# Performance work log

Measured on AMD Instinct MI355X. Metric: run time of the kernel, lower is better.

The kernel has to match this reference:

```python
import jax, jax.numpy as jnp
import numpy as np

N = 38333          # poi_len == number of graph nodes (forced by fc_layer input dim)
E = 38333 * 32     # edges, avg degree 32
VOCAB = 400 + 38333 + 1083   # cat_len + poi_len + user_len = 39816
EMB = (128 - 3) // 2         # 62
IN_DIM = EMB * 2 + 3         # 127
SLOPE = 0.01                 # LeakyReLU default negative_slope


def setup_inputs() -> dict:
    key = jax.random.key(0)
    ks = jax.random.split(key, 20)
    ids = jax.random.randint(ks[0], (N, 2), 0, VOCAB).astype(jnp.float32)
    feats = jax.random.uniform(ks[1], (N, 3), dtype=jnp.float32)
    x = jnp.concatenate([ids, feats], axis=1)                      # [N,5]
    edge_index = jax.random.randint(ks[2], (2, E), 0, N, dtype=jnp.int64)
    s = 0.05
    inp = {
        "x": x,
        "edge_index": edge_index,
        "emb": jax.random.normal(ks[3], (VOCAB, EMB), jnp.float32) * s,
        "W1": jax.random.normal(ks[4], (IN_DIM, 64), jnp.float32) * s,
        "b1": jnp.zeros((64,), jnp.float32),
        "W2": jax.random.normal(ks[5], (64, 32), jnp.float32) * s,
        "b2": jnp.zeros((32,), jnp.float32),
        "W3": jax.random.normal(ks[6], (32, 32), jnp.float32) * s,
        "b3": jnp.zeros((32,), jnp.float32),
        "W4": jax.random.normal(ks[7], (32, 32), jnp.float32) * s,
        "b4": jnp.zeros((32,), jnp.float32),
        "W5": jax.random.normal(ks[8], (32, 1), jnp.float32) * s,
        "b5": jnp.zeros((1,), jnp.float32),
        "Wf1": jax.random.normal(ks[9], (N, 128), jnp.float32) * s,
        "bf1": jnp.zeros((128,), jnp.float32),
        "Wf2": jax.random.normal(ks[10], (128, 128), jnp.float32) * s,
        "bf2": jnp.zeros((128,), jnp.float32),
    }
    return inp


def _forward(x, edge_index, emb, W1, b1, W2, b2, W3, b3, W4, b4, W5, b5, Wf1, bf1, Wf2, bf2):
    row, col = edge_index[0], edge_index[1]
    # GCN symmetric normalization with self-loops: deg includes the self-loop (+1)
    deg = jax.ops.segment_sum(jnp.ones((E,), x.dtype), col, num_segments=N) + 1.0
    dinv = jax.lax.rsqrt(deg)
    norm = dinv[row] * dinv[col]          # [E]
    self_norm = dinv * dinv               # [N]

    def gcn(h, W, b):
        hw = h @ W                         # [N,out]
        agg = jax.ops.segment_sum(hw[row] * norm[:, None], col, num_segments=N)
        return agg + hw * self_norm[:, None] + b

    lrelu = lambda z: jnp.where(z >= 0, z, SLOPE * z)

    ids = x[:, 0:2].astype(jnp.int32)
    h = jnp.concatenate([emb[ids].reshape(N, -1), x[:, 2:5]], axis=1)  # [N,127]
    h = lrelu(gcn(h, W1, b1))
    h = lrelu(gcn(h, W2, b2))
    t = gcn(h, W3, b3)
    h = lrelu(t) + t
    t = gcn(h, W4, b4)
    h = lrelu(t) + t
    h = lrelu(gcn(h, W5, b5))              # [N,1]
    v = h.reshape(-1)                      # [N] == poi_len
    o = jax.nn.relu(v @ Wf1 + bf1)
    o = jax.nn.relu(o @ Wf2 + bf2)
    return o


def reference(x, edge_index, emb, W1, b1, W2, b2, W3, b3, W4, b4, W5, b5, Wf1, bf1, Wf2, bf2):
    return _forward(x, edge_index, emb, W1, b1, W2, b2, W3, b3, W4, b4, W5, b5, Wf1, bf1, Wf2, bf2)
```

## Files before the change

kernel.cpp:

```cpp
#include <hip/hip_runtime.h>
#include <math.h>

#define SLOPE 0.01f
#define FC1_BLOCKS 512
#define NB 256
#define HBLK 256
#define BCHUNK 2048
#define F8SC 512.0f


static inline int cdiv_l(long a, int b) { return (int)((a + (long)b - 1) / (long)b); }

__device__ __forceinline__ unsigned short f2bf(float f) {
    union { float f; unsigned int i; } x; x.f = f;
    unsigned int i = x.i;
    i += 0x7fffu + ((i >> 16) & 1u);
    return (unsigned short)(i >> 16);
}
__device__ __forceinline__ float bf2f(unsigned short u) {
    union { unsigned int i; float f; } x; x.i = ((unsigned int)u) << 16;
    return x.f;
}
__device__ __forceinline__ float4 bf2f4(ushort4 u) {
    return make_float4(bf2f(u.x), bf2f(u.y), bf2f(u.z), bf2f(u.w));
}
__device__ __forceinline__ ushort4 f2bf4(float4 f) {
    return make_ushort4(f2bf(f.x), f2bf(f.y), f2bf(f.z), f2bf(f.w));
}
__device__ __forceinline__ float2 bfp2_to_f2(unsigned int u) {
    return make_float2(bf2f((unsigned short)(u & 0xffffu)),
                       bf2f((unsigned short)(u >> 16)));
}

__device__ __forceinline__ float4 fp8x4_to_f4(unsigned int u) {
    auto lo = __builtin_amdgcn_cvt_pk_f32_fp8(u, false);
    auto hi = __builtin_amdgcn_cvt_pk_f32_fp8(u, true);
    return make_float4(lo[0], lo[1], hi[0], hi[1]);
}
__device__ __forceinline__ unsigned int f4_to_fp8x4(float4 v) {
    unsigned int u = 0;
    u = __builtin_amdgcn_cvt_pk_fp8_f32(v.x, v.y, u, false);
    u = __builtin_amdgcn_cvt_pk_fp8_f32(v.z, v.w, u, true);
    return u;
}

__global__ void k_front(const int* __restrict__ col, int* __restrict__ bhist, int E, int S,
                        const float* __restrict__ x, const float* __restrict__ emb,
                        unsigned short* __restrict__ h0, int N,
                        const float* __restrict__ W1, float* __restrict__ W1p,
                        int h0Blocks) {
    int b = blockIdx.x;
    if (b < HBLK) {
        __shared__ int hist[NB];
        int t = threadIdx.x;
        if (t < NB) hist[t] = 0;
        __syncthreads();
        for (int e = b * 256 + t; e < E; e += HBLK * 256)
            atomicAdd(&hist[col[e] / S], 1);
        __syncthreads();
        if (t < NB) bhist[b * NB + t] = hist[t];
        return;
    }
    b -= HBLK;
    if (b < h0Blocks) {
        int idx = b * 256 + threadIdx.x;
        if (idx >= N * 32) return;
        int i = idx >> 5;
        int g = idx & 31;
        const float* xr = x + (long)i * 5;
        int id0 = (int)xr[0], id1 = (int)xr[1];
        const float* e0p = emb + (long)id0 * 62;
        const float* e1p = emb + (long)id1 * 62;
        float v[4];
#pragma unroll
        for (int kk = 0; kk < 4; ++kk) {
            int k = 4 * g + kk;
            float val;
            if (k < 62)       val = e0p[k];
            else if (k < 124) val = e1p[k - 62];
            else if (k < 127) val = xr[2 + (k - 124)];
            else              val = 0.f;
            v[kk] = val;
        }
        *(ushort4*)(h0 + (long)i * 128 + 4 * g) =
            make_ushort4(f2bf(v[0]), f2bf(v[1]), f2bf(v[2]), f2bf(v[3]));
        return;
    }
    b -= h0Blocks;
    {
        int idx = b * 256 + threadIdx.x;
        if (idx >= 128 * 64) return;
        int k = idx >> 6;
        W1p[idx] = (k < 127) ? W1[idx] : 0.f;
    }
}

__global__ void k_bscan(const int* __restrict__ bhist, int* __restrict__ gcur,
                        int* __restrict__ gstart) {
    __shared__ int sums[4][NB];
    __shared__ int sc[NB];
    int t = threadIdx.x;
    int colId = t & (NB - 1), part = t >> 8;
    int s = 0;
    for (int b = part * (HBLK / 4); b < (part + 1) * (HBLK / 4); ++b)
        s += bhist[b * NB + colId];
    sums[part][colId] = s;
    __syncthreads();
    if (t < NB) {
        int v = sums[0][t] + sums[1][t] + sums[2][t] + sums[3][t];
        sc[t] = v;
    }
    __syncthreads();
    int v = (t < NB) ? sc[t] : 0;
    for (int d = 1; d < NB; d <<= 1) {
        int u = (t < NB && t >= d) ? sc[t - d] : 0;
        __syncthreads();
        if (t < NB) sc[t] += u;
        __syncthreads();
    }
    if (t < NB) {
        int excl = sc[t] - v;
        gcur[t] = excl;
        gstart[t] = excl;
        if (t == NB - 1) gstart[NB] = sc[t];
    }
}

__global__ void k_bucket(const int* __restrict__ row, const int* __restrict__ col,
                         int* __restrict__ gcur, unsigned int* __restrict__ ebuf,
                         int E, int S) {
    __shared__ int hist[NB], base[NB], lcur[NB];
    int t = threadIdx.x;
    if (t < NB) { hist[t] = 0; lcur[t] = 0; }
    __syncthreads();
    int e0 = blockIdx.x * BCHUNK;
    int e1 = min(e0 + BCHUNK, E);
    for (int e = e0 + t; e < e1; e += blockDim.x)
        atomicAdd(&hist[col[e] / S], 1);
    __syncthreads();
    if (t < NB) base[t] = hist[t] ? atomicAdd(&gcur[t], hist[t]) : 0;
    __syncthreads();
    for (int e = e0 + t; e < e1; e += blockDim.x) {
        int c = col[e], r = row[e];
        int b = c / S;
        int p = base[b] + atomicAdd(&lcur[b], 1);
        ebuf[p] = ((unsigned)c << 16) | (unsigned)r;
    }
}

__global__ void k_sortb(const unsigned int* __restrict__ ebuf,
                        const int* __restrict__ gstart,
                        int* __restrict__ off, float* __restrict__ dinv,
                        unsigned short* __restrict__ srcs, int N, int S, int E) {
    __shared__ int cntl[NB];
    __shared__ int lcur[NB];
    int b = blockIdx.x, t = threadIdx.x;
    int base_node = b * S;
    int nNodes = min(S, N - base_node);
    int start = gstart[b], end = gstart[b + 1];
    if (t < S) cntl[t] = 0;
    __syncthreads();
    for (int e = start + t; e < end; e += blockDim.x)
        atomicAdd(&cntl[(int)(ebuf[e] >> 16) - base_node], 1);
    __syncthreads();
    int myc = (t < S) ? cntl[t] : 0;
    for (int d = 1; d < S; d <<= 1) {
        int u = (t < S && t >= d) ? cntl[t - d] : 0;
        __syncthreads();
        if (t < S) cntl[t] += u;
        __syncthreads();
    }
    if (t < nNodes) {
        int excl = cntl[t] - myc;
        int node = base_node + t;
        off[node] = start + excl;
        dinv[node] = (float)(1.0 / sqrt((double)myc + 1.0));
        lcur[t] = excl;
    }
    if (b == NB - 1 && t == 0) off[N] = E;
    __syncthreads();
    for (int e = start + t; e < end; e += blockDim.x) {
        unsigned p = ebuf[e];
        int cl = (int)(p >> 16) - base_node;
        int pos = start + atomicAdd(&lcur[cl], 1);
        srcs[pos] = (unsigned short)(p & 0xFFFFu);
    }
}

__global__ void k_hw_rb8(const unsigned short* __restrict__ h, int ld,
                         const float* __restrict__ W,
                         const float* __restrict__ dinv, unsigned char* __restrict__ out,
                         int N) {
    constexpr int DIN = 128, DOUT = 64;
    constexpr int Q = DOUT / 4;
    int tid = blockIdx.x * blockDim.x + threadIdx.x;
    int G = (N + 3) >> 2;
    if (tid >= G * Q) return;
    int g = tid / Q;
    int q = tid % Q;
    int i0 = 4 * g;
    const ushort4* h0 = (const ushort4*)(h + (long)i0 * ld);
    const ushort4* h1 = (const ushort4*)(h + (long)(i0 + 1) * ld);
    const ushort4* h2 = (const ushort4*)(h + (long)(i0 + 2) * ld);
    const ushort4* h3 = (const ushort4*)(h + (long)(i0 + 3) * ld);
    const float* wp = W + 4 * q;
    float4 acc0 = make_float4(0.f, 0.f, 0.f, 0.f);
    float4 acc1 = acc0, acc2 = acc0, acc3 = acc0;
#pragma unroll 4
    for (int kk = 0; kk < DIN / 4; ++kk) {
        float4 a0 = bf2f4(h0[kk]), a1 = bf2f4(h1[kk]);
        float4 a2 = bf2f4(h2[kk]), a3 = bf2f4(h3[kk]);
        float4 w0 = *(const float4*)(wp + (long)(4 * kk)     * DOUT);
        float4 w1 = *(const float4*)(wp + (long)(4 * kk + 1) * DOUT);
        float4 w2 = *(const float4*)(wp + (long)(4 * kk + 2) * DOUT);
        float4 w3 = *(const float4*)(wp + (long)(4 * kk + 3) * DOUT);
        acc0.x += a0.x * w0.x + a0.y * w1.x + a0.z * w2.x + a0.w * w3.x;
        acc0.y += a0.x * w0.y + a0.y * w1.y + a0.z * w2.y + a0.w * w3.y;
        acc0.z += a0.x * w0.z + a0.y * w1.z + a0.z * w2.z + a0.w * w3.z;
        acc0.w += a0.x * w0.w + a0.y * w1.w + a0.z * w2.w + a0.w * w3.w;
        acc1.x += a1.x * w0.x + a1.y * w1.x + a1.z * w2.x + a1.w * w3.x;
        acc1.y += a1.x * w0.y + a1.y * w1.y + a1.z * w2.y + a1.w * w3.y;
        acc1.z += a1.x * w0.z + a1.y * w1.z + a1.z * w2.z + a1.w * w3.z;
        acc1.w += a1.x * w0.w + a1.y * w1.w + a1.z * w2.w + a1.w * w3.w;
        acc2.x += a2.x * w0.x + a2.y * w1.x + a2.z * w2.x + a2.w * w3.x;
        acc2.y += a2.x * w0.y + a2.y * w1.y + a2.z * w2.y + a2.w * w3.y;
        acc2.z += a2.x * w0.z + a2.y * w1.z + a2.z * w2.z + a2.w * w3.z;
        acc2.w += a2.x * w0.w + a2.y * w1.w + a2.z * w2.w + a2.w * w3.w;
        acc3.x += a3.x * w0.x + a3.y * w1.x + a3.z * w2.x + a3.w * w3.x;
        acc3.y += a3.x * w0.y + a3.y * w1.y + a3.z * w2.y + a3.w * w3.y;
        acc3.z += a3.x * w0.z + a3.y * w1.z + a3.z * w2.z + a3.w * w3.z;
        acc3.w += a3.x * w0.w + a3.y * w1.w + a3.z * w2.w + a3.w * w3.w;
    }
    float d0 = dinv[i0] * F8SC, d1 = dinv[i0 + 1] * F8SC;
    float d2 = dinv[i0 + 2] * F8SC, d3 = dinv[i0 + 3] * F8SC;
    acc0.x *= d0; acc0.y *= d0; acc0.z *= d0; acc0.w *= d0;
    acc1.x *= d1; acc1.y *= d1; acc1.z *= d1; acc1.w *= d1;
    acc2.x *= d2; acc2.y *= d2; acc2.z *= d2; acc2.w *= d2;
    acc3.x *= d3; acc3.y *= d3; acc3.z *= d3; acc3.w *= d3;
    unsigned char* op = out + (long)i0 * DOUT + 4 * q;
    *(unsigned int*)(op) = f4_to_fp8x4(acc0);
    if (i0 + 1 < N) *(unsigned int*)(op + DOUT)     = f4_to_fp8x4(acc1);
    if (i0 + 2 < N) *(unsigned int*)(op + 2 * DOUT) = f4_to_fp8x4(acc2);
    if (i0 + 3 < N) *(unsigned int*)(op + 3 * DOUT) = f4_to_fp8x4(acc3);
}

__global__ void k_fused64_fp8(const int* __restrict__ off,
                              const unsigned short* __restrict__ srcs,
                              const float* __restrict__ dinv,
                              const unsigned char* __restrict__ hin,
                              const float* __restrict__ bg,
                              const float* __restrict__ W,
                              unsigned short* __restrict__ hwsOut, int N) {
    constexpr int DG = 64, QG = 16, NPB = 16;
    __shared__ float hrow[NPB][DG + 4];
    int t = threadIdx.x;
    int n = t / QG, q = t % QG;
    int c = blockIdx.x * NPB + n;
    const unsigned int* hp = (const unsigned int*)hin;
    if (c < N) {
        int e0 = off[c], e1 = off[c + 1];
        float dc = dinv[c] * (1.0f / F8SC);
        float4 acc = fp8x4_to_f4(hp[((long)c << 4) + q]);
        int e = e0;
        for (; e + 7 < e1; e += 8) {
            int r0 = srcs[e],     r1 = srcs[e + 1], r2 = srcs[e + 2], r3 = srcs[e + 3];
            int r4 = srcs[e + 4], r5 = srcs[e + 5], r6 = srcs[e + 6], r7 = srcs[e + 7];
            float4 v0 = fp8x4_to_f4(hp[((long)r0 << 4) + q]);
            float4 v1 = fp8x4_to_f4(hp[((long)r1 << 4) + q]);
            float4 v2 = fp8x4_to_f4(hp[((long)r2 << 4) + q]);
            float4 v3 = fp8x4_to_f4(hp[((long)r3 << 4) + q]);
            float4 v4 = fp8x4_to_f4(hp[((long)r4 << 4) + q]);
            float4 v5 = fp8x4_to_f4(hp[((long)r5 << 4) + q]);
            float4 v6 = fp8x4_to_f4(hp[((long)r6 << 4) + q]);
            float4 v7 = fp8x4_to_f4(hp[((long)r7 << 4) + q]);
            acc.x += (v0.x + v1.x) + (v2.x + v3.x);
            acc.y += (v0.y + v1.y) + (v2.y + v3.y);
            acc.z += (v0.z + v1.z) + (v2.z + v3.z);
            acc.w += (v0.w + v1.w) + (v2.w + v3.w);
            acc.x += (v4.x + v5.x) + (v6.x + v7.x);
            acc.y += (v4.y + v5.y) + (v6.y + v7.y);
            acc.z += (v4.z + v5.z) + (v6.z + v7.z);
            acc.w += (v4.w + v5.w) + (v6.w + v7.w);
        }
        for (; e + 3 < e1; e += 4) {
            int r0 = srcs[e], r1 = srcs[e + 1], r2 = srcs[e + 2], r3 = srcs[e + 3];
            float4 v0 = fp8x4_to_f4(hp[((long)r0 << 4) + q]);
            float4 v1 = fp8x4_to_f4(hp[((long)r1 << 4) + q]);
            float4 v2 = fp8x4_to_f4(hp[((long)r2 << 4) + q]);
            float4 v3 = fp8x4_to_f4(hp[((long)r3 << 4) + q]);
            acc.x += (v0.x + v1.x) + (v2.x + v3.x);
            acc.y += (v0.y + v1.y) + (v2.y + v3.y);
            acc.z += (v0.z + v1.z) + (v2.z + v3.z);
            acc.w += (v0.w + v1.w) + (v2.w + v3.w);
        }
        for (; e < e1; ++e) {
            int r = srcs[e];
            float4 v = fp8x4_to_f4(hp[((long)r << 4) + q]);
            acc.x += v.x; acc.y += v.y; acc.z += v.z; acc.w += v.w;
        }
        float4 bb = *(const float4*)(bg + 4 * q);
        float t0 = acc.x * dc + bb.x, t1 = acc.y * dc + bb.y;
        float t2 = acc.z * dc + bb.z, t3 = acc.w * dc + bb.w;
        float4 res;
        res.x = (t0 >= 0.f) ? t0 : SLOPE * t0;
        res.y = (t1 >= 0.f) ? t1 : SLOPE * t1;
        res.z = (t2 >= 0.f) ? t2 : SLOPE * t2;
        res.w = (t3 >= 0.f) ? t3 : SLOPE * t3;
        *(float4*)&hrow[n][4 * q] = res;
    }
    __syncthreads();
    int n2 = t >> 3;
    int q2 = t & 7;
    if (n2 < NPB) {
        int c2 = blockIdx.x * NPB + n2;
        if (c2 < N) {
            const float* wp = W + 4 * q2;
            float4 acc = make_float4(0.f, 0.f, 0.f, 0.f);
#pragma unroll
            for (int kk = 0; kk < DG / 4; ++kk) {
                float4 a = *(const float4*)&hrow[n2][4 * kk];
                float4 w0 = *(const float4*)(wp + (long)(4 * kk)     * 32);
                float4 w1 = *(const float4*)(wp + (long)(4 * kk + 1) * 32);
                float4 w2 = *(const float4*)(wp + (long)(4 * kk + 2) * 32);
                float4 w3 = *(const float4*)(wp + (long)(4 * kk + 3) * 32);
                acc.x += a.x * w0.x + a.y * w1.x + a.z * w2.x + a.w * w3.x;
                acc.y += a.x * w0.y + a.y * w1.y + a.z * w2.y + a.w * w3.y;
                acc.z += a.x * w0.z + a.y * w1.z + a.z * w2.z + a.w * w3.z;
                acc.w += a.x * w0.w + a.y * w1.w + a.z * w2.w + a.w * w3.w;
            }
            float di = dinv[c2];
            acc.x *= di; acc.y *= di; acc.z *= di; acc.w *= di;
            *(ushort4*)(hwsOut + (long)c2 * 32 + 4 * q2) = f2bf4(acc);
        }
    }
}

__global__ void k_fused32w(const int* __restrict__ off,
                           const unsigned short* __restrict__ srcs,
                           const float* __restrict__ dinv,
                           const unsigned short* __restrict__ hin,
                           const float* __restrict__ bg, int mode,
                           const float* __restrict__ W,
                           unsigned short* __restrict__ hwsOut, int N) {
    constexpr int DG = 32, QG = 16, NPB = 16;
    __shared__ float hrow[NPB][DG + 4];
    int t = threadIdx.x;
    int n = t / QG, q = t % QG;
    int c = blockIdx.x * NPB + n;
    const unsigned int* hp = (const unsigned int*)hin;
    if (c < N) {
        int e0 = off[c], e1 = off[c + 1];
        float dc = dinv[c];
        float2 acc = bfp2_to_f2(hp[((long)c << 4) + q]);
        int e = e0;
        for (; e + 7 < e1; e += 8) {
            int r0 = srcs[e],     r1 = srcs[e + 1], r2 = srcs[e + 2], r3 = srcs[e + 3];
            int r4 = srcs[e + 4], r5 = srcs[e + 5], r6 = srcs[e + 6], r7 = srcs[e + 7];
            float2 v0 = bfp2_to_f2(hp[((long)r0 << 4) + q]);
            float2 v1 = bfp2_to_f2(hp[((long)r1 << 4) + q]);
            float2 v2 = bfp2_to_f2(hp[((long)r2 << 4) + q]);
            float2 v3 = bfp2_to_f2(hp[((long)r3 << 4) + q]);
            float2 v4 = bfp2_to_f2(hp[((long)r4 << 4) + q]);
            float2 v5 = bfp2_to_f2(hp[((long)r5 << 4) + q]);
            float2 v6 = bfp2_to_f2(hp[((long)r6 << 4) + q]);
            float2 v7 = bfp2_to_f2(hp[((long)r7 << 4) + q]);
            acc.x += (v0.x + v1.x) + (v2.x + v3.x) + (v4.x + v5.x) + (v6.x + v7.x);
            acc.y += (v0.y + v1.y) + (v2.y + v3.y) + (v4.y + v5.y) + (v6.y + v7.y);
        }
        for (; e + 3 < e1; e += 4) {
            int r0 = srcs[e], r1 = srcs[e + 1], r2 = srcs[e + 2], r3 = srcs[e + 3];
            float2 v0 = bfp2_to_f2(hp[((long)r0 << 4) + q]);
            float2 v1 = bfp2_to_f2(hp[((long)r1 << 4) + q]);
            float2 v2 = bfp2_to_f2(hp[((long)r2 << 4) + q]);
            float2 v3 = bfp2_to_f2(hp[((long)r3 << 4) + q]);
            acc.x += (v0.x + v1.x) + (v2.x + v3.x);
            acc.y += (v0.y + v1.y) + (v2.y + v3.y);
        }
        for (; e < e1; ++e) {
            int r = srcs[e];
            float2 v = bfp2_to_f2(hp[((long)r << 4) + q]);
            acc.x += v.x; acc.y += v.y;
        }
        float b0 = bg[2 * q], b1v = bg[2 * q + 1];
        float t0 = acc.x * dc + b0, t1 = acc.y * dc + b1v;
        float2 res;
        if (mode == 0) {
            res.x = (t0 >= 0.f) ? t0 : SLOPE * t0;
            res.y = (t1 >= 0.f) ? t1 : SLOPE * t1;
        } else {
            res.x = (t0 >= 0.f) ? 2.f * t0 : (1.f + SLOPE) * t0;
            res.y = (t1 >= 0.f) ? 2.f * t1 : (1.f + SLOPE) * t1;
        }
        *(float2*)&hrow[n][2 * q] = res;
    }
    __syncthreads();
    int n2 = t >> 3;
    int q2 = t & 7;
    if (n2 < NPB) {
        int c2 = blockIdx.x * NPB + n2;
        if (c2 < N) {
            const float* wp = W + 4 * q2;
            float4 acc = make_float4(0.f, 0.f, 0.f, 0.f);
#pragma unroll
            for (int kk = 0; kk < DG / 4; ++kk) {
                float4 a = *(const float4*)&hrow[n2][4 * kk];
                float4 w0 = *(const float4*)(wp + (long)(4 * kk)     * 32);
                float4 w1 = *(const float4*)(wp + (long)(4 * kk + 1) * 32);
                float4 w2 = *(const float4*)(wp + (long)(4 * kk + 2) * 32);
                float4 w3 = *(const float4*)(wp + (long)(4 * kk + 3) * 32);
                acc.x += a.x * w0.x + a.y * w1.x + a.z * w2.x + a.w * w3.x;
                acc.y += a.x * w0.y + a.y * w1.y + a.z * w2.y + a.w * w3.y;
                acc.z += a.x * w0.z + a.y * w1.z + a.z * w2.z + a.w * w3.z;
                acc.w += a.x * w0.w + a.y * w1.w + a.z * w2.w + a.w * w3.w;
            }
            float di = dinv[c2];
            acc.x *= di; acc.y *= di; acc.z *= di; acc.w *= di;
            *(ushort4*)(hwsOut + (long)c2 * 32 + 4 * q2) = f2bf4(acc);
        }
    }
}

__global__ void k_fused_last_w(const int* __restrict__ off,
                               const unsigned short* __restrict__ srcs,
                               const float* __restrict__ dinv,
                               const unsigned short* __restrict__ hin,
                               const float* __restrict__ bg,
                               const float* __restrict__ W5,
                               float* __restrict__ hwsOut, int N) {
    constexpr int DG = 32, QG = 16, NPB = 16;
    __shared__ float hrow[NPB][DG + 4];
    int t = threadIdx.x;
    int n = t / QG, q = t % QG;
    int c = blockIdx.x * NPB + n;
    const unsigned int* hp = (const unsigned int*)hin;
    if (c < N) {
        int e0 = off[c], e1 = off[c + 1];
        float dc = dinv[c];
        float2 acc = bfp2_to_f2(hp[((long)c << 4) + q]);
        int e = e0;
        for (; e + 7 < e1; e += 8) {
            int r0 = srcs[e],     r1 = srcs[e + 1], r2 = srcs[e + 2], r3 = srcs[e + 3];
            int r4 = srcs[e + 4], r5 = srcs[e + 5], r6 = srcs[e + 6], r7 = srcs[e + 7];
            float2 v0 = bfp2_to_f2(hp[((long)r0 << 4) + q]);
            float2 v1 = bfp2_to_f2(hp[((long)r1 << 4) + q]);
            float2 v2 = bfp2_to_f2(hp[((long)r2 << 4) + q]);
            float2 v3 = bfp2_to_f2(hp[((long)r3 << 4) + q]);
            float2 v4 = bfp2_to_f2(hp[((long)r4 << 4) + q]);
            float2 v5 = bfp2_to_f2(hp[((long)r5 << 4) + q]);
            float2 v6 = bfp2_to_f2(hp[((long)r6 << 4) + q]);
            float2 v7 = bfp2_to_f2(hp[((long)r7 << 4) + q]);
            acc.x += (v0.x + v1.x) + (v2.x + v3.x) + (v4.x + v5.x) + (v6.x + v7.x);
            acc.y += (v0.y + v1.y) + (v2.y + v3.y) + (v4.y + v5.y) + (v6.y + v7.y);
        }
        for (; e + 3 < e1; e += 4) {
            int r0 = srcs[e], r1 = srcs[e + 1], r2 = srcs[e + 2], r3 = srcs[e + 3];
            float2 v0 = bfp2_to_f2(hp[((long)r0 << 4) + q]);
            float2 v1 = bfp2_to_f2(hp[((long)r1 << 4) + q]);
            float2 v2 = bfp2_to_f2(hp[((long)r2 << 4) + q]);
            float2 v3 = bfp2_to_f2(hp[((long)r3 << 4) + q]);
            acc.x += (v0.x + v1.x) + (v2.x + v3.x);
            acc.y += (v0.y + v1.y) + (v2.y + v3.y);
        }
        for (; e < e1; ++e) {
            int r = srcs[e];
            float2 v = bfp2_to_f2(hp[((long)r << 4) + q]);
            acc.x += v.x; acc.y += v.y;
        }
        float b0 = bg[2 * q], b1v = bg[2 * q + 1];
        float t0 = acc.x * dc + b0, t1 = acc.y * dc + b1v;
        float2 res;
        res.x = (t0 >= 0.f) ? 2.f * t0 : (1.f + SLOPE) * t0;
        res.y = (t1 >= 0.f) ? 2.f * t1 : (1.f + SLOPE) * t1;
        *(float2*)&hrow[n][2 * q] = res;
    }
    __syncthreads();
    if (t < NPB) {
        int c2 = blockIdx.x * NPB + t;
        if (c2 < N) {
            float acc = 0.f;
#pragma unroll
            for (int kk = 0; kk < 8; ++kk) {
                float4 a = *(const float4*)&hrow[t][4 * kk];
                acc += a.x * W5[4 * kk] + a.y * W5[4 * kk + 1]
                     + a.z * W5[4 * kk + 2] + a.w * W5[4 * kk + 3];
            }
            hwsOut[c2] = acc * dinv[c2];
        }
    }
}

__global__ void k_tail(const int* __restrict__ off,
                       const unsigned short* __restrict__ srcs,
                       const float* __restrict__ dinv, const float* __restrict__ hws,
                       const float* __restrict__ b5,
                       const float* __restrict__ Wf1, double* __restrict__ part,
                       int N, int chunk) {
    __shared__ float Vl[96];
    int bl = blockIdx.x, t = threadIdx.x;
    int i0 = bl * chunk;
    int i1 = min(i0 + chunk, N);
    int cnt = i1 - i0;
    if (t < cnt) {
        int c = i0 + t;
        int e0 = off[c], e1 = off[c + 1];
        float acc = hws[c];
        float a1 = 0.f, a2 = 0.f, a3 = 0.f;
        int e = e0;
        for (; e + 3 < e1; e += 4) {
            acc += hws[srcs[e]];
            a1  += hws[srcs[e + 1]];
            a2  += hws[srcs[e + 2]];
            a3  += hws[srcs[e + 3]];
        }
        for (; e < e1; ++e) acc += hws[srcs[e]];
        float tt = (acc + a1 + a2 + a3) * dinv[c] + b5[0];
        Vl[t] = (tt >= 0.f) ? tt : SLOPE * tt;
    }
    __syncthreads();
    int j = t;
    double a0 = 0.0, a1 = 0.0, a2 = 0.0, a3 = 0.0;
    int i = 0;
    for (; i + 3 < cnt; i += 4) {
        a0 += (double)Vl[i]     * (double)Wf1[(long)(i0 + i)     * 128 + j];
        a1 += (double)Vl[i + 1] * (double)Wf1[(long)(i0 + i + 1) * 128 + j];
        a2 += (double)Vl[i + 2] * (double)Wf1[(long)(i0 + i + 2) * 128 + j];
        a3 += (double)Vl[i + 3] * (double)Wf1[(long)(i0 + i + 3) * 128 + j];
    }
    for (; i < cnt; ++i)
        a0 += (double)Vl[i] * (double)Wf1[(long)(i0 + i) * 128 + j];
    part[bl * 128 + j] = (a0 + a1) + (a2 + a3);
}

__global__ void k_fc1b(const double* __restrict__ part, const float* __restrict__ bf1,
                       float* __restrict__ o1) {
    __shared__ double red[256];
    int j = blockIdx.x;
    int t = threadIdx.x;
    double a = part[t * 128 + j] + part[(t + 256) * 128 + j];
    red[t] = a;
    __syncthreads();
    for (int s = 128; s > 0; s >>= 1) {
        if (t < s) red[t] += red[t + s];
        __syncthreads();
    }
    if (t == 0) {
        double v = red[0] + (double)bf1[j];
        o1[j] = (float)((v > 0.0) ? v : 0.0);
    }
}

__global__ void k_fc2(const float* __restrict__ o1, const float* __restrict__ Wf2,
                      const float* __restrict__ bf2, float* __restrict__ out) {
    __shared__ double red[128];
    int j = blockIdx.x;
    int k = threadIdx.x;
    red[k] = (double)o1[k] * (double)Wf2[(long)k * 128 + j];
    __syncthreads();
    for (int s = 64; s > 0; s >>= 1) {
        if (k < s) red[k] += red[k + s];
        __syncthreads();
    }
    if (k == 0) {
        double u = red[0] + (double)bf2[j];
        out[j] = (float)((u > 0.0) ? u : 0.0);
    }
}

extern "C" void kernel_launch(void* const* d_in, const int* in_sizes, int n_in,
                              void* d_out, int out_size, void* d_ws, size_t ws_size,
                              hipStream_t stream) {
    const float* x   = (const float*)d_in[0];
    const int*   ei  = (const int*)d_in[1];
    const float* emb = (const float*)d_in[2];
    const float* W1  = (const float*)d_in[3];
    const float* b1  = (const float*)d_in[4];
    const float* W2  = (const float*)d_in[5];
    const float* b2  = (const float*)d_in[6];
    const float* W3  = (const float*)d_in[7];
    const float* b3  = (const float*)d_in[8];
    const float* W4  = (const float*)d_in[9];
    const float* b4  = (const float*)d_in[10];
    const float* W5  = (const float*)d_in[11];
    const float* b5  = (const float*)d_in[12];
    const float* Wf1 = (const float*)d_in[13];
    const float* bf1 = (const float*)d_in[14];
    const float* Wf2 = (const float*)d_in[15];
    const float* bf2 = (const float*)d_in[16];

    const int N = in_sizes[0] / 5;
    const int E = in_sizes[1] / 2;
    const int* row = ei;
    const int* col = ei + E;
    const int S = (N + NB - 1) / NB;
    const int Np = N + 4;

    char* ws = (char*)d_ws;
    size_t off_b = 0;
    auto alloc = [&](size_t bytes) -> void* {
        void* p = ws + off_b;
        off_b += (bytes + 255) & ~(size_t)255;
        return p;
    };
    int*   offcsr = (int*)alloc((size_t)(N + 1) * sizeof(int));
    int*   bhist  = (int*)alloc((size_t)HBLK * NB * sizeof(int));
    int*   gcur   = (int*)alloc((size_t)NB * sizeof(int));
    int*   gstart = (int*)alloc((size_t)(NB + 1) * sizeof(int));
    unsigned short* srcs = (unsigned short*)alloc((size_t)E * sizeof(unsigned short));
    unsigned int* ebuf = (unsigned int*)alloc((size_t)E * sizeof(unsigned int));
    float* dinv   = (float*)alloc((size_t)Np * sizeof(float));
    float* W1p    = (float*)alloc((size_t)128 * 64 * sizeof(float));
    unsigned short* H0   = (unsigned short*)alloc((size_t)Np * 128 * sizeof(unsigned short));
    unsigned char*  X64f8 = (unsigned char*)alloc((size_t)Np * 64 * sizeof(unsigned char));
    unsigned short* X32a = (unsigned short*)alloc((size_t)Np * 32 * sizeof(unsigned short));
    unsigned short* X32b = (unsigned short*)alloc((size_t)Np * 32 * sizeof(unsigned short));
    unsigned short* X32c = (unsigned short*)alloc((size_t)Np * 32 * sizeof(unsigned short));
    float* HWSf   = (float*)alloc((size_t)Np * sizeof(float));
    double* part  = (double*)alloc((size_t)FC1_BLOCKS * 128 * sizeof(double));
    float* O1     = (float*)alloc(128 * sizeof(float));

    int h0Blocks  = cdiv_l((long)N * 32, 256);
    int padBlocks = cdiv_l(128 * 64, 256);
    k_front<<<HBLK + h0Blocks + padBlocks, 256, 0, stream>>>(
        col, bhist, E, S, x, emb, H0, N, W1, W1p, h0Blocks);

    k_bscan<<<1, 1024, 0, stream>>>(bhist, gcur, gstart);
    k_bucket<<<cdiv_l(E, BCHUNK), 256, 0, stream>>>(row, col, gcur, ebuf, E, S);
    k_sortb<<<NB, 1024, 0, stream>>>(ebuf, gstart, offcsr, dinv, srcs, N, S, E);

    {
        int G = (N + 3) / 4;
        k_hw_rb8<<<cdiv_l((long)G * 16, 256), 256, 0, stream>>>(
            H0, 128, W1p, dinv, X64f8, N);
    }
    k_fused64_fp8<<<cdiv_l(N, 16), 256, 0, stream>>>(
        offcsr, srcs, dinv, X64f8, b1, W2, X32a, N);
    k_fused32w<<<cdiv_l(N, 16), 256, 0, stream>>>(
        offcsr, srcs, dinv, X32a, b2, 0, W3, X32b, N);
    k_fused32w<<<cdiv_l(N, 16), 256, 0, stream>>>(
        offcsr, srcs, dinv, X32b, b3, 1, W4, X32c, N);
    k_fused_last_w<<<cdiv_l(N, 16), 256, 0, stream>>>(
        offcsr, srcs, dinv, X32c, b4, W5, HWSf, N);

    int chunk = (N + FC1_BLOCKS - 1) / FC1_BLOCKS;
    k_tail<<<FC1_BLOCKS, 128, 0, stream>>>(
        offcsr, srcs, dinv, HWSf, b5, Wf1, part, N, chunk);
    k_fc1b<<<128, 256, 0, stream>>>(part, bf1, O1);
    k_fc2<<<128, 128, 0, stream>>>(O1, Wf2, bf2, (float*)d_out);
}
```

Baseline: 268.4 us.

## Sort nodes by in-degree to balance edge work across aggregation wavefronts

Builds a degree histogram during CSR construction, scans it, and scatters node ids into a degree-sorted permutation. The four fused GCN aggregation kernels then process nodes in that order, so the 16 nodes sharing a block have similar edge counts. This targets divergence and tail imbalance inside wavefronts. The cost is two extra small kernel launches, an extra indirection per node, and less locality for output writes and self-row reads, since neighbouring threads now touch non-contiguous node ids.

```diff
diff --git a/kernel.cpp b/kernel.cpp
--- a/kernel.cpp
+++ b/kernel.cpp
@@ -96,10 +96,11 @@
 }
 
 __global__ void k_bscan(const int* __restrict__ bhist, int* __restrict__ gcur,
-                        int* __restrict__ gstart) {
+                        int* __restrict__ gstart, int* __restrict__ dhist) {
     __shared__ int sums[4][NB];
     __shared__ int sc[NB];
     int t = threadIdx.x;
+    if (t < 256) dhist[t] = 0;
     int colId = t & (NB - 1), part = t >> 8;
     int s = 0;
     for (int b = part * (HBLK / 4); b < (part + 1) * (HBLK / 4); ++b)
@@ -151,7 +152,8 @@
 __global__ void k_sortb(const unsigned int* __restrict__ ebuf,
                         const int* __restrict__ gstart,
                         int* __restrict__ off, float* __restrict__ dinv,
-                        unsigned short* __restrict__ srcs, int N, int S, int E) {
+                        unsigned short* __restrict__ srcs,
+                        int* __restrict__ dhist, int N, int S, int E) {
     __shared__ int cntl[NB];
     __shared__ int lcur[NB];
     int b = blockIdx.x, t = threadIdx.x;
@@ -176,6 +178,7 @@
         off[node] = start + excl;
         dinv[node] = (float)(1.0 / sqrt((double)myc + 1.0));
         lcur[t] = excl;
+        atomicAdd(&dhist[min(myc, 255)], 1);
     }
     if (b == NB - 1 && t == 0) off[N] = E;
     __syncthreads();
@@ -185,6 +188,30 @@
         int pos = start + atomicAdd(&lcur[cl], 1);
         srcs[pos] = (unsigned short)(p & 0xFFFFu);
     }
+}
+
+__global__ void k_dscan(const int* __restrict__ dhist, int* __restrict__ dcur) {
+    __shared__ int sc[256];
+    int t = threadIdx.x;
+    int v = dhist[t];
+    sc[t] = v;
+    __syncthreads();
+    for (int d = 1; d < 256; d <<= 1) {
+        int u = (t >= d) ? sc[t - d] : 0;
+        __syncthreads();
+        sc[t] += u;
+        __syncthreads();
+    }
+    dcur[t] = sc[t] - v;
+}
+
+__global__ void k_dscatter(const int* __restrict__ off, int* __restrict__ dcur,
+                           unsigned short* __restrict__ perm, int N) {
+    int n = blockIdx.x * 256 + threadIdx.x;
+    if (n >= N) return;
+    int deg = off[n + 1] - off[n];
+    int pos = atomicAdd(&dcur[min(deg, 255)], 1);
+    perm[pos] = (unsigned short)n;
 }
 
 __global__ void k_hw_rb8(const unsigned short* __restrict__ h, int ld,
@@ -247,6 +274,7 @@
 __global__ void k_fused64_fp8(const int* __restrict__ off,
                               const unsigned short* __restrict__ srcs,
                               const float* __restrict__ dinv,
+                              const unsigned short* __restrict__ perm,
                               const unsigned char* __restrict__ hin,
                               const float* __restrict__ bg,
                               const float* __restrict__ W,
@@ -255,9 +283,10 @@
     __shared__ float hrow[NPB][DG + 4];
     int t = threadIdx.x;
     int n = t / QG, q = t % QG;
-    int c = blockIdx.x * NPB + n;
+    int ci = blockIdx.x * NPB + n;
     const unsigned int* hp = (const unsigned int*)hin;
-    if (c < N) {
+    if (ci < N) {
+        int c = perm[ci];
         int e0 = off[c], e1 = off[c + 1];
         float dc = dinv[c] * (1.0f / F8SC);
         float4 acc = fp8x4_to_f4(hp[((long)c << 4) + q]);
@@ -312,8 +341,9 @@
     int n2 = t >> 3;
     int q2 = t & 7;
     if (n2 < NPB) {
-        int c2 = blockIdx.x * NPB + n2;
-        if (c2 < N) {
+        int c2i = blockIdx.x * NPB + n2;
+        if (c2i < N) {
+            int c2 = perm[c2i];
             const float* wp = W + 4 * q2;
             float4 acc = make_float4(0.f, 0.f, 0.f, 0.f);
 #pragma unroll
@@ -338,6 +368,7 @@
 __global__ void k_fused32w(const int* __restrict__ off,
                            const unsigned short* __restrict__ srcs,
                            const float* __restrict__ dinv,
+                           const unsigned short* __restrict__ perm,
                            const unsigned short* __restrict__ hin,
                            const float* __restrict__ bg, int mode,
                            const float* __restrict__ W,
@@ -346,9 +377,10 @@
     __shared__ float hrow[NPB][DG + 4];
     int t = threadIdx.x;
     int n = t / QG, q = t % QG;
-    int c = blockIdx.x * NPB + n;
+    int ci = blockIdx.x * NPB + n;
     const unsigned int* hp = (const unsigned int*)hin;
-    if (c < N) {
+    if (ci < N) {
+        int c = perm[ci];
         int e0 = off[c], e1 = off[c + 1];
         float dc = dinv[c];
         float2 acc = bfp2_to_f2(hp[((long)c << 4) + q]);
@@ -397,8 +429,9 @@
     int n2 = t >> 3;
     int q2 = t & 7;
     if (n2 < NPB) {
-        int c2 = blockIdx.x * NPB + n2;
-        if (c2 < N) {
+        int c2i = blockIdx.x * NPB + n2;
+        if (c2i < N) {
+            int c2 = perm[c2i];
             const float* wp = W + 4 * q2;
             float4 acc = make_float4(0.f, 0.f, 0.f, 0.f);
 #pragma unroll
@@ -423,6 +456,7 @@
 __global__ void k_fused_last_w(const int* __restrict__ off,
                                const unsigned short* __restrict__ srcs,
                                const float* __restrict__ dinv,
+                               const unsigned short* __restrict__ perm,
                                const unsigned short* __restrict__ hin,
                                const float* __restrict__ bg,
                                const float* __restrict__ W5,
@@ -431,9 +465,10 @@
     __shared__ float hrow[NPB][DG + 4];
     int t = threadIdx.x;
     int n = t / QG, q = t % QG;
-    int c = blockIdx.x * NPB + n;
+    int ci = blockIdx.x * NPB + n;
     const unsigned int* hp = (const unsigned int*)hin;
-    if (c < N) {
+    if (ci < N) {
+        int c = perm[ci];
         int e0 = off[c], e1 = off[c + 1];
         float dc = dinv[c];
         float2 acc = bfp2_to_f2(hp[((long)c << 4) + q]);
@@ -475,8 +510,9 @@
     }
     __syncthreads();
     if (t < NPB) {
-        int c2 = blockIdx.x * NPB + t;
-        if (c2 < N) {
+        int c2i = blockIdx.x * NPB + t;
+        if (c2i < N) {
+            int c2 = perm[c2i];
             float acc = 0.f;
 #pragma unroll
             for (int kk = 0; kk < 8; ++kk) {
@@ -605,6 +641,9 @@
     int*   bhist  = (int*)alloc((size_t)HBLK * NB * sizeof(int));
     int*   gcur   = (int*)alloc((size_t)NB * sizeof(int));
     int*   gstart = (int*)alloc((size_t)(NB + 1) * sizeof(int));
+    int*   dhist  = (int*)alloc(256 * sizeof(int));
+    int*   dcur   = (int*)alloc(256 * sizeof(int));
+    unsigned short* perm = (unsigned short*)alloc((size_t)Np * sizeof(unsigned short));
     unsigned short* srcs = (unsigned short*)alloc((size_t)E * sizeof(unsigned short));
     unsigned int* ebuf = (unsigned int*)alloc((size_t)E * sizeof(unsigned int));
     float* dinv   = (float*)alloc((size_t)Np * sizeof(float));
@@ -623,9 +662,11 @@
     k_front<<<HBLK + h0Blocks + padBlocks, 256, 0, stream>>>(
         col, bhist, E, S, x, emb, H0, N, W1, W1p, h0Blocks);
 
-    k_bscan<<<1, 1024, 0, stream>>>(bhist, gcur, gstart);
+    k_bscan<<<1, 1024, 0, stream>>>(bhist, gcur, gstart, dhist);
     k_bucket<<<cdiv_l(E, BCHUNK), 256, 0, stream>>>(row, col, gcur, ebuf, E, S);
-    k_sortb<<<NB, 1024, 0, stream>>>(ebuf, gstart, offcsr, dinv, srcs, N, S, E);
+    k_sortb<<<NB, 1024, 0, stream>>>(ebuf, gstart, offcsr, dinv, srcs, dhist, N, S, E);
+    k_dscan<<<1, 256, 0, stream>>>(dhist, dcur);
+    k_dscatter<<<cdiv_l(N, 256), 256, 0, stream>>>(offcsr, dcur, perm, N);
 
     {
         int G = (N + 3) / 4;
@@ -633,13 +674,13 @@
             H0, 128, W1p, dinv, X64f8, N);
     }
     k_fused64_fp8<<<cdiv_l(N, 16), 256, 0, stream>>>(
-        offcsr, srcs, dinv, X64f8, b1, W2, X32a, N);
+        offcsr, srcs, dinv, perm, X64f8, b1, W2, X32a, N);
     k_fused32w<<<cdiv_l(N, 16), 256, 0, stream>>>(
-        offcsr, srcs, dinv, X32a, b2, 0, W3, X32b, N);
+        offcsr, srcs, dinv, perm, X32a, b2, 0, W3, X32b, N);
     k_fused32w<<<cdiv_l(N, 16), 256, 0, stream>>>(
-        offcsr, srcs, dinv, X32b, b3, 1, W4, X32c, N);
+        offcsr, srcs, dinv, perm, X32b, b3, 1, W4, X32c, N);
     k_fused_last_w<<<cdiv_l(N, 16), 256, 0, stream>>>(
-        offcsr, srcs, dinv, X32c, b4, W5, HWSf, N);
+        offcsr, srcs, dinv, perm, X32c, b4, W5, HWSf, N);
 
     int chunk = (N + FC1_BLOCKS - 1) / FC1_BLOCKS;
     k_tail<<<FC1_BLOCKS, 128, 0, stream>>>(
```

Result: slower. 406.4 us (+51.4%).
